# Optimization experiments

Measured on AMD Instinct MI355X. Metric: run time of the kernel, lower is better.

## Reference

```python
import jax, jax.numpy as jnp
import numpy as np
import math

B, L, S = 4, 4096, 4096
D_MODEL, N_HEADS, FACTOR = 1024, 16, 5
D_K = D_MODEL // N_HEADS
SCALE = 1.0 / math.sqrt(D_K)
SAMPLE_K = min(FACTOR * int(math.log(L)), S)  # 40
N_TOP = max(1, min(FACTOR * int(math.log(L)), L))  # 40


def setup_inputs() -> dict:
    key = jax.random.key(0)
    ks = jax.random.split(key, 12)
    f = lambda k, shp: jax.random.normal(k, shp, dtype=jnp.float32)
    w = lambda k: f(k, (D_MODEL, D_MODEL)) * 0.02
    return {
        "queries": f(ks[0], (B, L, D_MODEL)),
        "keys": f(ks[1], (B, S, D_MODEL)),
        "values": f(ks[2], (B, S, D_MODEL)),
        "Wq": w(ks[3]), "bq": jnp.zeros((D_MODEL,), jnp.float32),
        "Wk": w(ks[4]), "bk": jnp.zeros((D_MODEL,), jnp.float32),
        "Wv": w(ks[5]), "bv": jnp.zeros((D_MODEL,), jnp.float32),
        "Wo": w(ks[6]), "bo": jnp.zeros((D_MODEL,), jnp.float32),
        "index_sample": jax.random.randint(ks[7], (SAMPLE_K,), 0, S),
    }


def _proj(x, W, b):
    # torch nn.Linear: x @ W.T + b, then split heads -> (B, H, seq, d_k)
    y = x @ W.T + b
    Bx, T, _ = x.shape
    return y.reshape(Bx, T, N_HEADS, D_K).transpose(0, 2, 1, 3)


def reference(queries, keys, values, Wq, bq, Wk, bk, Wv, bv, Wo, bo, index_sample):
    Q = _proj(queries, Wq, bq)   # (B, H, L, D_K)
    K = _proj(keys, Wk, bk)      # (B, H, S, D_K)
    V = _proj(values, Wv, bv)    # (B, H, S, D_K)

    # sampled QK scoring: gather sample_k keys, score all queries against them
    K_sample = K[:, :, index_sample, :]                          # (B, H, sample_k, D_K)
    QK_s = jnp.einsum('bhld,bhsd->bhls', Q, K_sample)            # (B, H, L, sample_k)
    M = QK_s.max(axis=-1) - QK_s.mean(axis=-1)                   # sparsity measure (B, H, L)
    _, M_top = jax.lax.top_k(M, N_TOP)                           # (B, H, n_top)

    # gather top queries, dense attention over full K for those queries only
    Q_red = jnp.take_along_axis(Q, M_top[..., None], axis=2)     # (B, H, n_top, D_K)
    attn = jax.nn.softmax(jnp.einsum('bhtd,bhsd->bhts', Q_red, K) * SCALE, axis=-1)
    context = jnp.einsum('bhts,bhsd->bhtd', attn, V)             # (B, H, n_top, D_K)

    # scatter context back into zero-initialized full tensor
    bi = jnp.arange(B)[:, None, None]
    hi = jnp.arange(N_HEADS)[None, :, None]
    full = jnp.zeros((B, N_HEADS, L, D_K), context.dtype).at[bi, hi, M_top].set(context)

    out = full.transpose(0, 2, 1, 3).reshape(B, L, D_MODEL)
    return out @ Wo.T + bo
```

## Files before the change

kernel.cpp:

```cpp
#include <hip/hip_runtime.h>


#define NTOP 40
#define NSAMP 40
#define SCALE 0.125f
#define SPLIT 16
#define KEYS_PER_SPLIT 256
#define CHUNK 64
#define NCHUNK 4

#define Q_OFF    0ull
#define K_OFF    16777216ull
#define V_OFF    33554432ull
#define M_OFF    50331648ull
#define MTOP_OFF 50593792ull
#define WOT_OFF  50597888ull
#define CTXP_OFF 51646464ull
#define MLP_OFF  55840768ull
#define CTX_OFF  55971840ull

typedef __attribute__((ext_vector_type(8))) short short8;
typedef __attribute__((ext_vector_type(4))) float floatx4;

__device__ inline unsigned short bf16_rne(float f) {
  unsigned u = __float_as_uint(f);
  unsigned r = (u + 0x7fffu + ((u >> 16) & 1u)) >> 16;
  return (unsigned short)r;
}

__global__ __launch_bounds__(256) void split_bf16(
    const float* __restrict__ x, unsigned short* __restrict__ hi,
    unsigned short* __restrict__ lo, int n4) {
  int i = blockIdx.x * 256 + threadIdx.x;
  if (i >= n4) return;
  float4 v = ((const float4*)x)[i];
  ushort4 h, l;
  {
    h.x = bf16_rne(v.x);
    float hf = __uint_as_float((unsigned)h.x << 16);
    l.x = bf16_rne(v.x - hf);
  }
  {
    h.y = bf16_rne(v.y);
    float hf = __uint_as_float((unsigned)h.y << 16);
    l.y = bf16_rne(v.y - hf);
  }
  {
    h.z = bf16_rne(v.z);
    float hf = __uint_as_float((unsigned)h.z << 16);
    l.z = bf16_rne(v.z - hf);
  }
  {
    h.w = bf16_rne(v.w);
    float hf = __uint_as_float((unsigned)h.w << 16);
    l.w = bf16_rne(v.w - hf);
  }
  ((ushort4*)hi)[i] = h;
  ((ushort4*)lo)[i] = l;
}

__device__ inline void gl_lds16(const void* g, void* l) {
  __builtin_amdgcn_global_load_lds(
      (const __attribute__((address_space(1))) void*)g,
      (__attribute__((address_space(3))) void*)l, 16, 0, 0);
}

__global__ __launch_bounds__(256) void proj_gemm_mfma(
    const unsigned short* __restrict__ Xh, const unsigned short* __restrict__ Xl,
    const unsigned short* __restrict__ Wh, const unsigned short* __restrict__ Wl,
    const float* __restrict__ bias, float* __restrict__ Out) {
  __shared__ unsigned short As[128 * 32];
  __shared__ unsigned short Bs[128 * 32];
  const int t = threadIdx.x;
  const int lane = t & 63;
  const int w = t >> 6;
  const int m0 = blockIdx.x * 128;
  const int n0 = blockIdx.y * 128;

  const int sr = t >> 2;
  const int sc = (t & 3) * 8;
  char* AsB = (char*)As;
  char* BsB = (char*)Bs;
  const int ldsW = w * 1024;

  const int frow = lane & 15;
  const int koct = lane >> 4;
  const int m_off = (w & 1) * 64;
  const int n_off = (w >> 1) * 64;

  floatx4 acc[4][4] = {};

  const unsigned short* Asrc[3] = {Xh, Xl, Xh};
  const unsigned short* Bsrc[3] = {Wh, Wh, Wl};

  for (int pass = 0; pass < 3; ++pass) {
    const unsigned short* Ap = Asrc[pass];
    const unsigned short* Bp = Bsrc[pass];
    for (int k0 = 0; k0 < 1024; k0 += 32) {
      __syncthreads();
      gl_lds16(&Ap[(size_t)(m0 + sr) * 1024 + k0 + sc], AsB + ldsW);
      gl_lds16(&Ap[(size_t)(m0 + 64 + sr) * 1024 + k0 + sc], AsB + 4096 + ldsW);
      gl_lds16(&Bp[(size_t)(n0 + sr) * 1024 + k0 + sc], BsB + ldsW);
      gl_lds16(&Bp[(size_t)(n0 + 64 + sr) * 1024 + k0 + sc], BsB + 4096 + ldsW);
      __syncthreads();
      short8 af[4], bf[4];
#pragma unroll
      for (int mt = 0; mt < 4; ++mt)
        af[mt] = *(const short8*)(AsB + ((m_off + mt * 16 + frow) * 32 + koct * 8) * 2);
#pragma unroll
      for (int nt = 0; nt < 4; ++nt)
        bf[nt] = *(const short8*)(BsB + ((n_off + nt * 16 + frow) * 32 + koct * 8) * 2);
#pragma unroll
      for (int mt = 0; mt < 4; ++mt)
#pragma unroll
        for (int nt = 0; nt < 4; ++nt)
          acc[mt][nt] = __builtin_amdgcn_mfma_f32_16x16x32_bf16(
              af[mt], bf[nt], acc[mt][nt], 0, 0, 0);
    }
  }

#pragma unroll
  for (int nt = 0; nt < 4; ++nt) {
    const int n_g = n0 + n_off + nt * 16 + frow;
    const float bv = bias[n_g];
    const int h = n_g >> 6, d = n_g & 63;
#pragma unroll
    for (int mt = 0; mt < 4; ++mt) {
#pragma unroll
      for (int r = 0; r < 4; ++r) {
        const int m_g = m0 + m_off + mt * 16 + koct * 4 + r;
        const int b = m_g >> 12, l = m_g & 4095;
        Out[(((size_t)(b * 16 + h)) * 4096 + l) * 64 + d] = acc[mt][nt][r] + bv;
      }
    }
  }
}

__global__ __launch_bounds__(256) void transpose1024(
    const float* __restrict__ A, float* __restrict__ AT) {
  __shared__ float tile[64][68];
  const int t = threadIdx.x;
  const int x0 = blockIdx.x * 64;
  const int y0 = blockIdx.y * 64;
  const int tr = t >> 4;
  const int tc = (t & 15) * 4;
#pragma unroll
  for (int i = 0; i < 4; ++i) {
    int r = tr + i * 16;
    float4 v = *(const float4*)&A[(size_t)(y0 + r) * 1024 + x0 + tc];
    *(float4*)&tile[r][tc] = v;
  }
  __syncthreads();
#pragma unroll
  for (int i = 0; i < 4; ++i) {
    int r = tr + i * 16;
    float4 v;
    v.x = tile[tc + 0][r];
    v.y = tile[tc + 1][r];
    v.z = tile[tc + 2][r];
    v.w = tile[tc + 3][r];
    *(float4*)&AT[(size_t)(x0 + r) * 1024 + y0 + tc] = v;
  }
}

__global__ __launch_bounds__(256) void sample_scores(
    const float* __restrict__ Q, const float* __restrict__ K,
    const int* __restrict__ samp, float* __restrict__ M) {
  __shared__ float Ks[NSAMP * 64];
  const int bh = blockIdx.y;
  const int t = threadIdx.x;
#pragma unroll
  for (int i = 0; i < 10; ++i) {
    int e = i * 256 + t;
    int s = e >> 6, d = e & 63;
    Ks[e] = K[((size_t)bh * 4096 + samp[s]) * 64 + d];
  }
  __syncthreads();
  const int l = blockIdx.x * 256 + t;
  const float* qp = &Q[((size_t)bh * 4096 + l) * 64];
  float4 q[16];
#pragma unroll
  for (int i = 0; i < 16; ++i) q[i] = *(const float4*)&qp[i * 4];
  float mx = -1e30f, sum = 0.f;
#pragma unroll
  for (int s = 0; s < NSAMP; ++s) {
    float acc = 0.f;
#pragma unroll
    for (int i = 0; i < 16; ++i) {
      float4 kv = *(const float4*)&Ks[s * 64 + i * 4];
      acc = fmaf(q[i].x, kv.x, acc);
      acc = fmaf(q[i].y, kv.y, acc);
      acc = fmaf(q[i].z, kv.z, acc);
      acc = fmaf(q[i].w, kv.w, acc);
    }
    mx = fmaxf(mx, acc);
    sum += acc;
  }
  M[(size_t)bh * 4096 + l] = mx - sum * (1.f / 40.f);
}

__global__ __launch_bounds__(256) void topk40(
    const float* __restrict__ M, int* __restrict__ Mtop) {
  __shared__ unsigned long long keys[4096];
  __shared__ unsigned long long red[256];
  const int bh = blockIdx.x;
  const int t = threadIdx.x;
#pragma unroll
  for (int i = 0; i < 16; ++i) {
    int idx = i * 256 + t;
    float f = M[(size_t)bh * 4096 + idx];
    unsigned int u = __float_as_uint(f);
    u = (u & 0x80000000u) ? ~u : (u | 0x80000000u);
    keys[idx] = (((unsigned long long)u) << 32) | (unsigned long long)(4095 - idx);
  }
  __syncthreads();
  for (int it = 0; it < NTOP; ++it) {
    unsigned long long best = 0;
#pragma unroll
    for (int i = 0; i < 16; ++i) {
      unsigned long long v = keys[i * 256 + t];
      best = v > best ? v : best;
    }
    red[t] = best;
    __syncthreads();
    for (int s = 128; s > 0; s >>= 1) {
      if (t < s) {
        unsigned long long o = red[t + s];
        if (o > red[t]) red[t] = o;
      }
      __syncthreads();
    }
    int idx = 4095 - (int)(red[0] & 0xFFFFFFFFull);
    if (t == 0) {
      Mtop[bh * NTOP + it] = idx;
      keys[idx] = 0;
    }
    __syncthreads();
  }
}

__global__ __launch_bounds__(256) void init_out(
    const float* __restrict__ bo, float* __restrict__ out) {
  const int t = threadIdx.x;
  const float4* bo4 = (const float4*)bo;
  float4* o4 = (float4*)out;
#pragma unroll
  for (int rep = 0; rep < 4; ++rep) {
    size_t idx = (size_t)rep * 1048576 + (size_t)blockIdx.x * 256 + t;
    o4[idx] = bo4[idx & 255];
  }
}

__global__ __launch_bounds__(256) void flash_attn(
    const float* __restrict__ Q, const float* __restrict__ K,
    const float* __restrict__ V, const int* __restrict__ Mtop,
    float* __restrict__ ctx_part, float* __restrict__ ml_part) {
  __shared__ float Qs[NTOP * 64];
  __shared__ float Ks[64 * 64];
  __shared__ float Vs[64 * 64];
  __shared__ float Sb[64 * 41];
  __shared__ int topIdx[NTOP];
  const int t = threadIdx.x;
  const int lane = t & 63;
  const int w = t >> 6;
  const int split = blockIdx.x;
  const int bh = blockIdx.y;

  if (t < NTOP) topIdx[t] = Mtop[bh * NTOP + t];
  __syncthreads();
  for (int i = t; i < NTOP * 16; i += 256) {
    int r = i >> 4, c4 = i & 15;
    *(float4*)&Qs[r * 64 + c4 * 4] =
        *(const float4*)&Q[(((size_t)bh) * 4096 + topIdx[r]) * 64 + c4 * 4];
  }

  const float* Kb = K + (size_t)bh * 4096 * 64;
  const float* Vb = V + (size_t)bh * 4096 * 64;
  const int key0 = split * KEYS_PER_SPLIT;
  const int d0 = w * 16;
  const int s_in_row = lane & 15;
  const int lrow = lane >> 4;

  float m_r = -1e30f, l_r = 0.f;
  float4 acc0 = make_float4(0.f, 0.f, 0.f, 0.f);
  float4 acc1 = acc0, acc2 = acc0, acc3 = acc0;

  for (int c = 0; c < NCHUNK; ++c) {
    __syncthreads();
    const int jbase = key0 + c * CHUNK;
#pragma unroll
    for (int n = 0; n < 4; ++n) {
      const int slot0 = n * 256 + w * 64;
      const int j = (slot0 >> 4) + lrow;
      const int d4 = (s_in_row - j) & 15;
      gl_lds16(&Kb[(size_t)(jbase + j) * 64 + d4 * 4], (char*)Ks + slot0 * 16);
      gl_lds16(&Vb[(size_t)jbase * 64 + (size_t)(slot0 + lane) * 4],
               (char*)Vs + slot0 * 16);
    }
    __syncthreads();

    float4 kr[16];
#pragma unroll
    for (int i = 0; i < 16; ++i)
      kr[i] = *(const float4*)&Ks[(lane * 16 + ((i + lane) & 15)) * 4];
#pragma unroll
    for (int rr = 0; rr < 10; ++rr) {
      const int r = w * 10 + rr;
      const float* qrow = &Qs[r * 64];
      float s = 0.f;
#pragma unroll
      for (int i = 0; i < 16; ++i) {
        float4 q4 = *(const float4*)&qrow[i * 4];
        s = fmaf(q4.x, kr[i].x, s);
        s = fmaf(q4.y, kr[i].y, s);
        s = fmaf(q4.z, kr[i].z, s);
        s = fmaf(q4.w, kr[i].w, s);
      }
      Sb[lane * 41 + r] = s * SCALE;
    }
    __syncthreads();

    if (lane < NTOP) {
      float sv[64];
      float cm = -1e30f;
#pragma unroll
      for (int j2 = 0; j2 < 64; ++j2) {
        sv[j2] = Sb[j2 * 41 + lane];
        cm = fmaxf(cm, sv[j2]);
      }
      const float nm = fmaxf(m_r, cm);
      const float alpha = __expf(m_r - nm);
      m_r = nm;
      l_r *= alpha;
      acc0.x *= alpha; acc0.y *= alpha; acc0.z *= alpha; acc0.w *= alpha;
      acc1.x *= alpha; acc1.y *= alpha; acc1.z *= alpha; acc1.w *= alpha;
      acc2.x *= alpha; acc2.y *= alpha; acc2.z *= alpha; acc2.w *= alpha;
      acc3.x *= alpha; acc3.y *= alpha; acc3.z *= alpha; acc3.w *= alpha;
#pragma unroll
      for (int j2 = 0; j2 < 64; ++j2) {
        const float p = __expf(sv[j2] - nm);
        l_r += p;
        const float* vrow = &Vs[j2 * 64 + d0];
        float4 v0 = *(const float4*)&vrow[0];
        float4 v1 = *(const float4*)&vrow[4];
        float4 v2 = *(const float4*)&vrow[8];
        float4 v3 = *(const float4*)&vrow[12];
        acc0.x = fmaf(p, v0.x, acc0.x); acc0.y = fmaf(p, v0.y, acc0.y);
        acc0.z = fmaf(p, v0.z, acc0.z); acc0.w = fmaf(p, v0.w, acc0.w);
        acc1.x = fmaf(p, v1.x, acc1.x); acc1.y = fmaf(p, v1.y, acc1.y);
        acc1.z = fmaf(p, v1.z, acc1.z); acc1.w = fmaf(p, v1.w, acc1.w);
        acc2.x = fmaf(p, v2.x, acc2.x); acc2.y = fmaf(p, v2.y, acc2.y);
        acc2.z = fmaf(p, v2.z, acc2.z); acc2.w = fmaf(p, v2.w, acc2.w);
        acc3.x = fmaf(p, v3.x, acc3.x); acc3.y = fmaf(p, v3.y, acc3.y);
        acc3.z = fmaf(p, v3.z, acc3.z); acc3.w = fmaf(p, v3.w, acc3.w);
      }
    }
  }

  if (lane < NTOP) {
    size_t pbase = (((size_t)split * 64 + bh) * 64 + lane) * 64 + d0;
    *(float4*)&ctx_part[pbase + 0] = acc0;
    *(float4*)&ctx_part[pbase + 4] = acc1;
    *(float4*)&ctx_part[pbase + 8] = acc2;
    *(float4*)&ctx_part[pbase + 12] = acc3;
  }
  if (w == 0) {
    size_t mb = (((size_t)split * 64 + bh) * 64 + lane) * 2;
    ml_part[mb + 0] = m_r;
    ml_part[mb + 1] = l_r;
  }
}

__global__ __launch_bounds__(256) void combine_ctx(
    const float* __restrict__ ctx_part, const float* __restrict__ ml_part,
    float* __restrict__ ctx) {
  const int bh = blockIdx.x;
  const int t = threadIdx.x;
  const int r = t & 63;
  const int dg = t >> 6;
  if (r >= NTOP) return;
  float mt = -1e30f;
#pragma unroll
  for (int s = 0; s < SPLIT; ++s)
    mt = fmaxf(mt, ml_part[(((size_t)s * 64 + bh) * 64 + r) * 2]);
  float Lt = 0.f;
  float4 a0 = make_float4(0.f, 0.f, 0.f, 0.f);
  float4 a1 = a0, a2 = a0, a3 = a0;
  const int d0 = dg * 16;
#pragma unroll
  for (int s = 0; s < SPLIT; ++s) {
    size_t mb = (((size_t)s * 64 + bh) * 64 + r) * 2;
    float ms = ml_part[mb], ls = ml_part[mb + 1];
    float wgt = __expf(ms - mt);
    Lt = fmaf(wgt, ls, Lt);
    size_t pb = (((size_t)s * 64 + bh) * 64 + r) * 64 + d0;
    float4 c0 = *(const float4*)&ctx_part[pb + 0];
    float4 c1 = *(const float4*)&ctx_part[pb + 4];
    float4 c2 = *(const float4*)&ctx_part[pb + 8];
    float4 c3 = *(const float4*)&ctx_part[pb + 12];
    a0.x = fmaf(wgt, c0.x, a0.x); a0.y = fmaf(wgt, c0.y, a0.y);
    a0.z = fmaf(wgt, c0.z, a0.z); a0.w = fmaf(wgt, c0.w, a0.w);
    a1.x = fmaf(wgt, c1.x, a1.x); a1.y = fmaf(wgt, c1.y, a1.y);
    a1.z = fmaf(wgt, c1.z, a1.z); a1.w = fmaf(wgt, c1.w, a1.w);
    a2.x = fmaf(wgt, c2.x, a2.x); a2.y = fmaf(wgt, c2.y, a2.y);
    a2.z = fmaf(wgt, c2.z, a2.z); a2.w = fmaf(wgt, c2.w, a2.w);
    a3.x = fmaf(wgt, c3.x, a3.x); a3.y = fmaf(wgt, c3.y, a3.y);
    a3.z = fmaf(wgt, c3.z, a3.z); a3.w = fmaf(wgt, c3.w, a3.w);
  }
  float inv = 1.f / Lt;
  size_t ob = ((size_t)bh * NTOP + r) * 64 + d0;
  a0.x *= inv; a0.y *= inv; a0.z *= inv; a0.w *= inv;
  a1.x *= inv; a1.y *= inv; a1.z *= inv; a1.w *= inv;
  a2.x *= inv; a2.y *= inv; a2.z *= inv; a2.w *= inv;
  a3.x *= inv; a3.y *= inv; a3.z *= inv; a3.w *= inv;
  *(float4*)&ctx[ob + 0] = a0;
  *(float4*)&ctx[ob + 4] = a1;
  *(float4*)&ctx[ob + 8] = a2;
  *(float4*)&ctx[ob + 12] = a3;
}

__global__ __launch_bounds__(256) void scatter_out(
    const float* __restrict__ ctx, const int* __restrict__ Mtop,
    const float* __restrict__ WoT, float* __restrict__ out) {
  const int bx = blockIdx.x;
  const int bh = bx / NTOP;
  const int r = bx % NTOP;
  const int b = bh >> 4, h = bh & 15;
  const int t = threadIdx.x;
  __shared__ float crow[64];
  if (t < 16)
    *(float4*)&crow[t * 4] =
        *(const float4*)&ctx[((size_t)bh * NTOP + r) * 64 + t * 4];
  const int l = Mtop[bh * NTOP + r];
  __syncthreads();
  const int n0 = t * 4;
  float4 a = make_float4(0.f, 0.f, 0.f, 0.f);
#pragma unroll
  for (int d = 0; d < 64; ++d) {
    float cv = crow[d];
    float4 wv = *(const float4*)&WoT[(size_t)(h * 64 + d) * 1024 + n0];
    a.x = fmaf(cv, wv.x, a.x);
    a.y = fmaf(cv, wv.y, a.y);
    a.z = fmaf(cv, wv.z, a.z);
    a.w = fmaf(cv, wv.w, a.w);
  }
  float* orow = out + ((size_t)b * 4096 + l) * 1024 + n0;
  atomicAdd(&orow[0], a.x);
  atomicAdd(&orow[1], a.y);
  atomicAdd(&orow[2], a.z);
  atomicAdd(&orow[3], a.w);
}

extern "C" void kernel_launch(void* const* d_in, const int* in_sizes, int n_in,
                              void* d_out, int out_size, void* d_ws, size_t ws_size,
                              hipStream_t stream) {
  const float* queries = (const float*)d_in[0];
  const float* keys    = (const float*)d_in[1];
  const float* values  = (const float*)d_in[2];
  const float* Wq = (const float*)d_in[3];
  const float* bq = (const float*)d_in[4];
  const float* Wk = (const float*)d_in[5];
  const float* bk = (const float*)d_in[6];
  const float* Wv = (const float*)d_in[7];
  const float* bv = (const float*)d_in[8];
  const float* Wo = (const float*)d_in[9];
  const float* bo = (const float*)d_in[10];
  const int* samp = (const int*)d_in[11];
  float* out = (float*)d_out;
  float* ws = (float*)d_ws;

  float* Qw   = ws + Q_OFF;
  float* Kw   = ws + K_OFF;
  float* Vw   = ws + V_OFF;
  float* Mws  = ws + M_OFF;
  int*   Mtop = (int*)(ws + MTOP_OFF);
  float* WoT  = ws + WOT_OFF;
  float* ctxp = ws + CTXP_OFF;
  float* mlp  = ws + MLP_OFF;
  float* ctxf = ws + CTX_OFF;

  unsigned short* Xh = (unsigned short*)d_out;
  unsigned short* Xl = Xh + 16777216;
  unsigned short* Whi = (unsigned short*)(ws + CTXP_OFF);
  unsigned short* Wlo = Whi + 1048576;

  dim3 ggrid(128, 8);

  split_bf16<<<16384, 256, 0, stream>>>(queries, Xh, Xl, 4194304);
  split_bf16<<<1024, 256, 0, stream>>>(Wq, Whi, Wlo, 262144);
  proj_gemm_mfma<<<ggrid, 256, 0, stream>>>(Xh, Xl, Whi, Wlo, bq, Qw);

  split_bf16<<<16384, 256, 0, stream>>>(keys, Xh, Xl, 4194304);
  split_bf16<<<1024, 256, 0, stream>>>(Wk, Whi, Wlo, 262144);
  proj_gemm_mfma<<<ggrid, 256, 0, stream>>>(Xh, Xl, Whi, Wlo, bk, Kw);

  split_bf16<<<16384, 256, 0, stream>>>(values, Xh, Xl, 4194304);
  split_bf16<<<1024, 256, 0, stream>>>(Wv, Whi, Wlo, 262144);
  proj_gemm_mfma<<<ggrid, 256, 0, stream>>>(Xh, Xl, Whi, Wlo, bv, Vw);

  transpose1024<<<dim3(16, 16), 256, 0, stream>>>(Wo, WoT);
  sample_scores<<<dim3(16, 64), 256, 0, stream>>>(Qw, Kw, samp, Mws);
  topk40<<<64, 256, 0, stream>>>(Mws, Mtop);
  init_out<<<4096, 256, 0, stream>>>(bo, out);
  flash_attn<<<dim3(SPLIT, 64), 256, 0, stream>>>(Qw, Kw, Vw, Mtop, ctxp, mlp);
  combine_ctx<<<64, 256, 0, stream>>>(ctxp, mlp, ctxf);
  scatter_out<<<2560, 256, 0, stream>>>(ctxf, Mtop, WoT, out);
}
```

Before: 953.3 us.

## Swizzle GEMM LDS layout, batch weight splits, double attention key splits

XOR-swizzles the LDS column placement in the projection GEMM so the MFMA fragment reads avoid bank conflicts. Converts all three weight matrices to bf16 hi/lo in one launch instead of three. Doubles the flash-attention key split (32 splits of 128 keys) to raise parallelism, moving the partial context buffers into the output buffer. init_out now runs after the combine step so those partials can live there. This adds scratch-buffer aliasing that depends on launch order being kept.

```diff
diff --git a/kernel.cpp b/kernel.cpp
--- a/kernel.cpp
+++ b/kernel.cpp
@@ -4,10 +4,10 @@
 #define NTOP 40
 #define NSAMP 40
 #define SCALE 0.125f
-#define SPLIT 16
-#define KEYS_PER_SPLIT 256
+#define SPLIT 32
+#define KEYS_PER_SPLIT 128
 #define CHUNK 64
-#define NCHUNK 4
+#define NCHUNK 2
 
 #define Q_OFF    0ull
 #define K_OFF    16777216ull
@@ -15,8 +15,7 @@
 #define M_OFF    50331648ull
 #define MTOP_OFF 50593792ull
 #define WOT_OFF  50597888ull
-#define CTXP_OFF 51646464ull
-#define MLP_OFF  55840768ull
+#define WHL_OFF  51646464ull
 #define CTX_OFF  55971840ull
 
 typedef __attribute__((ext_vector_type(8))) short short8;
@@ -26,6 +25,13 @@
   unsigned u = __float_as_uint(f);
   unsigned r = (u + 0x7fffu + ((u >> 16) & 1u)) >> 16;
   return (unsigned short)r;
+}
+
+__device__ inline void split4(float4 v, ushort4& h, ushort4& l) {
+  h.x = bf16_rne(v.x); l.x = bf16_rne(v.x - __uint_as_float((unsigned)h.x << 16));
+  h.y = bf16_rne(v.y); l.y = bf16_rne(v.y - __uint_as_float((unsigned)h.y << 16));
+  h.z = bf16_rne(v.z); l.z = bf16_rne(v.z - __uint_as_float((unsigned)h.z << 16));
+  h.w = bf16_rne(v.w); l.w = bf16_rne(v.w - __uint_as_float((unsigned)h.w << 16));
 }
 
 __global__ __launch_bounds__(256) void split_bf16(
@@ -33,30 +39,23 @@
     unsigned short* __restrict__ lo, int n4) {
   int i = blockIdx.x * 256 + threadIdx.x;
   if (i >= n4) return;
-  float4 v = ((const float4*)x)[i];
   ushort4 h, l;
-  {
-    h.x = bf16_rne(v.x);
-    float hf = __uint_as_float((unsigned)h.x << 16);
-    l.x = bf16_rne(v.x - hf);
-  }
-  {
-    h.y = bf16_rne(v.y);
-    float hf = __uint_as_float((unsigned)h.y << 16);
-    l.y = bf16_rne(v.y - hf);
-  }
-  {
-    h.z = bf16_rne(v.z);
-    float hf = __uint_as_float((unsigned)h.z << 16);
-    l.z = bf16_rne(v.z - hf);
-  }
-  {
-    h.w = bf16_rne(v.w);
-    float hf = __uint_as_float((unsigned)h.w << 16);
-    l.w = bf16_rne(v.w - hf);
-  }
+  split4(((const float4*)x)[i], h, l);
   ((ushort4*)hi)[i] = h;
   ((ushort4*)lo)[i] = l;
+}
+
+__global__ __launch_bounds__(256) void splitW_bf16(
+    const float* __restrict__ W0, const float* __restrict__ W1,
+    const float* __restrict__ W2, unsigned short* __restrict__ hi,
+    unsigned short* __restrict__ lo) {
+  const int i = blockIdx.x * 256 + threadIdx.x;
+  const int s = blockIdx.y;
+  const float* W = (s == 0) ? W0 : (s == 1) ? W1 : W2;
+  ushort4 h, l;
+  split4(((const float4*)W)[i], h, l);
+  ((ushort4*)hi)[(size_t)s * 262144 + i] = h;
+  ((ushort4*)lo)[(size_t)s * 262144 + i] = l;
 }
 
 __device__ inline void gl_lds16(const void* g, void* l) {
@@ -78,13 +77,14 @@
   const int n0 = blockIdx.y * 128;
 
   const int sr = t >> 2;
-  const int sc = (t & 3) * 8;
+  const int sc = (((t & 3) ^ ((sr >> 1) & 3))) * 8;
   char* AsB = (char*)As;
   char* BsB = (char*)Bs;
   const int ldsW = w * 1024;
 
   const int frow = lane & 15;
   const int koct = lane >> 4;
+  const int koct2 = koct ^ ((frow >> 1) & 3);
   const int m_off = (w & 1) * 64;
   const int n_off = (w >> 1) * 64;
 
@@ -106,10 +106,10 @@
       short8 af[4], bf[4];
 #pragma unroll
       for (int mt = 0; mt < 4; ++mt)
-        af[mt] = *(const short8*)(AsB + ((m_off + mt * 16 + frow) * 32 + koct * 8) * 2);
+        af[mt] = *(const short8*)(AsB + ((m_off + mt * 16 + frow) * 32 + koct2 * 8) * 2);
 #pragma unroll
       for (int nt = 0; nt < 4; ++nt)
-        bf[nt] = *(const short8*)(BsB + ((n_off + nt * 16 + frow) * 32 + koct * 8) * 2);
+        bf[nt] = *(const short8*)(BsB + ((n_off + nt * 16 + frow) * 32 + koct2 * 8) * 2);
 #pragma unroll
       for (int mt = 0; mt < 4; ++mt)
 #pragma unroll
@@ -475,34 +475,36 @@
   float* Mws  = ws + M_OFF;
   int*   Mtop = (int*)(ws + MTOP_OFF);
   float* WoT  = ws + WOT_OFF;
-  float* ctxp = ws + CTXP_OFF;
-  float* mlp  = ws + MLP_OFF;
   float* ctxf = ws + CTX_OFF;
+
+  unsigned short* Whi = (unsigned short*)(ws + WHL_OFF);
+  unsigned short* Wlo = Whi + 3 * 1048576;
 
   unsigned short* Xh = (unsigned short*)d_out;
   unsigned short* Xl = Xh + 16777216;
-  unsigned short* Whi = (unsigned short*)(ws + CTXP_OFF);
-  unsigned short* Wlo = Whi + 1048576;
+  float* ctxp = (float*)d_out;
+  float* mlp  = (float*)d_out + 8388608;
 
   dim3 ggrid(128, 8);
 
+  splitW_bf16<<<dim3(1024, 3), 256, 0, stream>>>(Wq, Wk, Wv, Whi, Wlo);
+
   split_bf16<<<16384, 256, 0, stream>>>(queries, Xh, Xl, 4194304);
-  split_bf16<<<1024, 256, 0, stream>>>(Wq, Whi, Wlo, 262144);
   proj_gemm_mfma<<<ggrid, 256, 0, stream>>>(Xh, Xl, Whi, Wlo, bq, Qw);
 
   split_bf16<<<16384, 256, 0, stream>>>(keys, Xh, Xl, 4194304);
-  split_bf16<<<1024, 256, 0, stream>>>(Wk, Whi, Wlo, 262144);
-  proj_gemm_mfma<<<ggrid, 256, 0, stream>>>(Xh, Xl, Whi, Wlo, bk, Kw);
+  proj_gemm_mfma<<<ggrid, 256, 0, stream>>>(Xh, Xl, Whi + 1048576,
+                                            Wlo + 1048576, bk, Kw);
 
   split_bf16<<<16384, 256, 0, stream>>>(values, Xh, Xl, 4194304);
-  split_bf16<<<1024, 256, 0, stream>>>(Wv, Whi, Wlo, 262144);
-  proj_gemm_mfma<<<ggrid, 256, 0, stream>>>(Xh, Xl, Whi, Wlo, bv, Vw);
+  proj_gemm_mfma<<<ggrid, 256, 0, stream>>>(Xh, Xl, Whi + 2097152,
+                                            Wlo + 2097152, bv, Vw);
 
   transpose1024<<<dim3(16, 16), 256, 0, stream>>>(Wo, WoT);
   sample_scores<<<dim3(16, 64), 256, 0, stream>>>(Qw, Kw, samp, Mws);
   topk40<<<64, 256, 0, stream>>>(Mws, Mtop);
-  init_out<<<4096, 256, 0, stream>>>(bo, out);
   flash_attn<<<dim3(SPLIT, 64), 256, 0, stream>>>(Qw, Kw, Vw, Mtop, ctxp, mlp);
   combine_ctx<<<64, 256, 0, stream>>>(ctxp, mlp, ctxf);
+  init_out<<<4096, 256, 0, stream>>>(bo, out);
   scatter_out<<<2560, 256, 0, stream>>>(ctxf, Mtop, WoT, out);
 }
```

Measured after the change: 1.003 ms. +5.2%, slower.
